# Kernel optimization log

Hardware: AMD Instinct MI355X
Metric: run time of the kernel (lower is better)

Reference implementation:

```python
import jax, jax.numpy as jnp
import numpy as np

N = 50000      # nodes
E = 800000     # edges (avg degree 16)
F_IN = 128     # input features
HID = 64       # hidden per head
HEADS = 4      # heads per layer
G = 256        # graphs in batch
C = 10         # classes
ALPHA = 0.01   # leaky relu negative slope


def setup_inputs() -> dict:
    key = jax.random.key(0)
    ks = jax.random.split(key, 12)
    x = jax.random.normal(ks[0], (N, F_IN), dtype=jnp.float32)
    edge_index = jax.random.randint(ks[1], (2, E), 0, N, dtype=jnp.int32)
    batch = jnp.sort(jax.random.randint(ks[2], (N,), 0, G, dtype=jnp.int32))

    def glorot(k, shape):
        fan_in = shape[0] if len(shape) == 2 else int(np.prod(shape[1:]))
        return (jax.random.normal(k, shape, dtype=jnp.float32) / np.float32(np.sqrt(fan_in)))

    W1 = glorot(ks[3], (F_IN, HEADS * HID))
    a1_src = glorot(ks[4], (HEADS, HID))
    a1_dst = glorot(ks[5], (HEADS, HID))
    W2 = glorot(ks[6], (HEADS * HID, HEADS * HID))
    a2_src = glorot(ks[7], (HEADS, HID))
    a2_dst = glorot(ks[8], (HEADS, HID))
    lin_W = glorot(ks[9], (2 * HEADS * HID, C))
    lin_b = jnp.zeros((C,), dtype=jnp.float32)
    return {
        "x": x, "edge_index": edge_index, "batch": batch,
        "W1": W1, "a1_src": a1_src, "a1_dst": a1_dst,
        "W2": W2, "a2_src": a2_src, "a2_dst": a2_dst,
        "lin_W": lin_W, "lin_b": lin_b,
    }


def _gat_layer(x, src, dst, W, a_src, a_dst):
    """Multi-head GAT layer: edge softmax over incoming neighbors, concat heads, ELU."""
    n = x.shape[0]
    h, f = a_src.shape
    Wh = (x @ W).reshape(n, h, f)                       # [N,H,F]
    # per-node attention logits (decomposed GAT attention a^T [Wh_i || Wh_j])
    ls = jnp.einsum("nhf,hf->nh", Wh, a_src)            # [N,H]
    ld = jnp.einsum("nhf,hf->nh", Wh, a_dst)            # [N,H]
    e = jax.nn.leaky_relu(ls[src] + ld[dst], ALPHA)      # [E,H]
    # numerically-stable softmax over edges grouped by destination node
    m = jax.ops.segment_max(e, dst, num_segments=n)      # [N,H]
    m = jnp.where(jnp.isfinite(m), m, 0.0)
    p = jnp.exp(e - m[dst])                              # [E,H]
    z = jax.ops.segment_sum(p, dst, num_segments=n)      # [N,H]
    attn = p / (z[dst] + 1e-16)                          # [E,H]
    msg = Wh[src] * attn[:, :, None]                     # [E,H,F]
    out = jax.ops.segment_sum(msg, dst, num_segments=n)  # [N,H,F]
    return jax.nn.elu(out.reshape(n, h * f))


def reference(x, edge_index, batch, W1, a1_src, a1_dst, W2, a2_src, a2_dst, lin_W, lin_b):
    src, dst = edge_index[0], edge_index[1]
    x = _gat_layer(x, src, dst, W1, a1_src, a1_dst)
    x = _gat_layer(x, src, dst, W2, a2_src, a2_dst)
    # global max / mean pool per graph
    mx = jax.ops.segment_max(x, batch, num_segments=G)
    mx = jnp.where(jnp.isfinite(mx), mx, 0.0)
    s = jax.ops.segment_sum(x, batch, num_segments=G)
    cnt = jax.ops.segment_sum(jnp.ones((x.shape[0], 1), x.dtype), batch, num_segments=G)
    mean = s / jnp.maximum(cnt, 1.0)
    pooled = jnp.concatenate([mx, mean], axis=1)         # [G, 2*H*F]
    return pooled @ lin_W + lin_b                        # [G, C]
```

## Files before the change

### kernel.cpp

```cpp
#include <hip/hip_runtime.h>
#include <hip/hip_bf16.h>

#define NNODES 50000
#define NEDGES 800000
#define FIN    128
#define HID    64
#define HEADS  4
#define NGRAPH 256
#define NCLS   10
#define DTOT   256
#define ALPHA  0.01f
#define CAPLG  6
#define CAP    (1 << CAPLG)

typedef short bf16x8 __attribute__((ext_vector_type(8)));
typedef float f32x4  __attribute__((ext_vector_type(4)));

#define NB      ((NNODES + 255) / 256)
#define EB      ((NEDGES + 255) / 256)
#define XB      ((NNODES * FIN / 4 + 255) / 256)
#define W1B     (FIN * DTOT / 256)
#define W2B     (DTOT * DTOT / 256)

__device__ __forceinline__ ushort f2bf(float v) {
    return __bfloat16_as_ushort(__float2bfloat16(v));
}
__device__ __forceinline__ float blo(unsigned u) { return __uint_as_float(u << 16); }
__device__ __forceinline__ float bhi(unsigned u) { return __uint_as_float(u & 0xffff0000u); }

__global__ __launch_bounds__(256) void k_setup(const int* __restrict__ src, const int* __restrict__ dst,
                                               int* __restrict__ cursor, ushort* __restrict__ esrc,
                                               const int* __restrict__ batch, int* __restrict__ gstart,
                                               const float4* __restrict__ x4, ushort4* __restrict__ xbf4,
                                               const float* __restrict__ W1, ushort* __restrict__ W1t,
                                               const float* __restrict__ W2, ushort* __restrict__ W2t) {
    int b = blockIdx.x, t = threadIdx.x;
    if (b < EB) {
        int e = b * 256 + t;
        if (e < NEDGES) {
            int d = dst[e];
            int pos = atomicAdd(&cursor[d], 1);
            if (pos < CAP) esrc[(d << CAPLG) + pos] = (ushort)src[e];
        }
    } else if (b < EB + NB) {
        int i = (b - EB) * 256 + t;
        if (i >= NNODES) return;
        int bb = batch[i];
        if (i == 0) {
            for (int g = 0; g <= bb; ++g) gstart[g] = 0;
        } else {
            int pb = batch[i - 1];
            if (pb != bb) for (int g = pb + 1; g <= bb; ++g) gstart[g] = i;
        }
        if (i == NNODES - 1)
            for (int g = bb + 1; g <= NGRAPH; ++g) gstart[g] = NNODES;
    } else if (b < EB + NB + XB) {
        int i = (b - EB - NB) * 256 + t;
        if (i >= NNODES * FIN / 4) return;
        float4 v = x4[i];
        ushort4 o;
        o.x = f2bf(v.x); o.y = f2bf(v.y); o.z = f2bf(v.z); o.w = f2bf(v.w);
        xbf4[i] = o;
    } else if (b < EB + NB + XB + W1B) {
        int id = (b - EB - NB - XB) * 256 + t;
        int n = id & 255, k = id >> 8;
        W1t[n * FIN + (((k >> 3) ^ (n & 7)) << 3) + (k & 7)] = f2bf(W1[k * DTOT + n]);
    } else {
        int id = (b - EB - NB - XB - W1B) * 256 + t;
        int n = id & 255, k = id >> 8;
        W2t[n * DTOT + (((k >> 3) ^ (n & 7)) << 3) + (k & 7)] = f2bf(W2[k * DTOT + n]);
    }
}

template <int K>
__global__ __launch_bounds__(256) void k_gemm_mfma(const ushort* __restrict__ Abf,
                                                   const ushort* __restrict__ Bt,
                                                   ushort* __restrict__ Cbf,
                                                   float* __restrict__ ls,
                                                   float* __restrict__ ld_,
                                                   const float* __restrict__ a_src,
                                                   const float* __restrict__ a_dst,
                                                   int M) {
    __shared__ ushort Bl[128 * K];
    const int tid  = threadIdx.x;
    const int w    = tid >> 6;
    const int lane = tid & 63;
    const int l15  = lane & 15;
    const int quad = lane >> 4;
    const int m0 = blockIdx.y * 128;
    const int n0 = blockIdx.x * 128;
    const int hb = blockIdx.x * 2;

    {
        const uint4* sp = (const uint4*)(Bt + (size_t)n0 * K);
        uint4* dp = (uint4*)Bl;
#pragma unroll
        for (int idx = tid; idx < 128 * K / 8; idx += 256) dp[idx] = sp[idx];
    }
    __syncthreads();

    f32x4 acc[2][8];
#pragma unroll
    for (int mf = 0; mf < 2; ++mf)
#pragma unroll
        for (int nf = 0; nf < 8; ++nf)
            acc[mf][nf] = (f32x4){0.f, 0.f, 0.f, 0.f};

    const int rbase = m0 + w * 32;
    int rowA0 = rbase + l15;       if (rowA0 >= M) rowA0 = M - 1;
    int rowA1 = rbase + 16 + l15;  if (rowA1 >= M) rowA1 = M - 1;
    const ushort* pa0 = Abf + (size_t)rowA0 * K + quad * 8;
    const ushort* pa1 = Abf + (size_t)rowA1 * K + quad * 8;

#pragma unroll
    for (int ks = 0; ks < K / 32; ++ks) {
        bf16x8 a0 = *(const bf16x8*)(pa0 + ks * 32);
        bf16x8 a1 = *(const bf16x8*)(pa1 + ks * 32);
        bf16x8 bfr[8];
#pragma unroll
        for (int nf = 0; nf < 8; ++nf) {
            int n = nf * 16 + l15;
            int c = (ks * 4 + quad) ^ (n & 7);
            bfr[nf] = *(const bf16x8*)&Bl[n * K + (c << 3)];
        }
#pragma unroll
        for (int nf = 0; nf < 8; ++nf) {
            acc[0][nf] = __builtin_amdgcn_mfma_f32_16x16x32_bf16(a0, bfr[nf], acc[0][nf], 0, 0, 0);
            acc[1][nf] = __builtin_amdgcn_mfma_f32_16x16x32_bf16(a1, bfr[nf], acc[1][nf], 0, 0, 0);
        }
    }

    float as[8], ad[8];
#pragma unroll
    for (int nf = 0; nf < 8; ++nf) {
        int head = hb + (nf >> 2);
        as[nf] = a_src[head * HID + (nf & 3) * 16 + l15];
        ad[nf] = a_dst[head * HID + (nf & 3) * 16 + l15];
    }
#pragma unroll
    for (int mf = 0; mf < 2; ++mf) {
#pragma unroll
        for (int reg = 0; reg < 4; ++reg) {
            int row = rbase + mf * 16 + quad * 4 + reg;
            bool ok = row < M;
            if (ok) {
#pragma unroll
                for (int nf = 0; nf < 8; ++nf)
                    Cbf[(size_t)row * DTOT + n0 + nf * 16 + l15] = f2bf(acc[mf][nf][reg]);
            }
            float s0 = 0.f, d0 = 0.f, s1 = 0.f, d1 = 0.f;
#pragma unroll
            for (int nf = 0; nf < 4; ++nf) {
                s0 += acc[mf][nf][reg] * as[nf];
                d0 += acc[mf][nf][reg] * ad[nf];
                s1 += acc[mf][nf + 4][reg] * as[nf + 4];
                d1 += acc[mf][nf + 4][reg] * ad[nf + 4];
            }
#pragma unroll
            for (int off = 1; off < 16; off <<= 1) {
                s0 += __shfl_xor(s0, off);
                d0 += __shfl_xor(d0, off);
                s1 += __shfl_xor(s1, off);
                d1 += __shfl_xor(d1, off);
            }
            if (ok && l15 == 0) {
                ls[row * HEADS + hb]      = s0;
                ld_[row * HEADS + hb]     = d0;
                ls[row * HEADS + hb + 1]  = s1;
                ld_[row * HEADS + hb + 1] = d1;
            }
        }
    }
}

__global__ __launch_bounds__(256) void k_gat_aggr(const int* __restrict__ cnt,
                                                  const ushort* __restrict__ esrc,
                                                  const ushort* __restrict__ Whbf,
                                                  const float* __restrict__ ls,
                                                  const float* __restrict__ ld_,
                                                  ushort* __restrict__ out) {
    const int wv   = threadIdx.x >> 6;
    const int lane = threadIdx.x & 63;
    const int i    = blockIdx.x * 4 + wv;
    if (i >= NNODES) return;
    const int half = lane >> 5;
    const int l32  = lane & 31;
    const int h    = l32 >> 3;
    const int e0 = i << CAPLG;
    int deg = cnt[i]; if (deg > CAP) deg = CAP;
    const int e1 = e0 + deg;
    const float ldv = ld_[i * HEADS + h];

    float mx = -INFINITY;
    for (int e = e0 + (l32 & 7) + 8 * half; e < e1; e += 16)
        mx = fmaxf(mx, ls[(int)esrc[e] * HEADS + h]);
    mx = fmaxf(mx, __shfl_xor(mx, 1));
    mx = fmaxf(mx, __shfl_xor(mx, 2));
    mx = fmaxf(mx, __shfl_xor(mx, 4));
    mx = fmaxf(mx, __shfl_xor(mx, 32));
    float lvm = mx + ldv;
    const float M = lvm > 0.f ? lvm : ALPHA * lvm;

    float ac[8] = {};
    float z = 0.f;
    const int ch = 8 * l32;
    int e = e0 + half;
    for (; e + 6 < e1; e += 8) {
        int s0 = (int)esrc[e], s1 = (int)esrc[e + 2], s2 = (int)esrc[e + 4], s3 = (int)esrc[e + 6];
        float l0 = ls[s0 * HEADS + h] + ldv;
        float l1 = ls[s1 * HEADS + h] + ldv;
        float l2 = ls[s2 * HEADS + h] + ldv;
        float l3 = ls[s3 * HEADS + h] + ldv;
        uint4 u0 = *(const uint4*)&Whbf[(size_t)s0 * DTOT + ch];
        uint4 u1 = *(const uint4*)&Whbf[(size_t)s1 * DTOT + ch];
        uint4 u2 = *(const uint4*)&Whbf[(size_t)s2 * DTOT + ch];
        uint4 u3 = *(const uint4*)&Whbf[(size_t)s3 * DTOT + ch];
        float p0 = __expf((l0 > 0.f ? l0 : ALPHA * l0) - M);
        float p1 = __expf((l1 > 0.f ? l1 : ALPHA * l1) - M);
        float p2 = __expf((l2 > 0.f ? l2 : ALPHA * l2) - M);
        float p3 = __expf((l3 > 0.f ? l3 : ALPHA * l3) - M);
        z += p0 + p1 + p2 + p3;
        ac[0] = fmaf(p0, blo(u0.x), ac[0]); ac[1] = fmaf(p0, bhi(u0.x), ac[1]);
        ac[2] = fmaf(p0, blo(u0.y), ac[2]); ac[3] = fmaf(p0, bhi(u0.y), ac[3]);
        ac[4] = fmaf(p0, blo(u0.z), ac[4]); ac[5] = fmaf(p0, bhi(u0.z), ac[5]);
        ac[6] = fmaf(p0, blo(u0.w), ac[6]); ac[7] = fmaf(p0, bhi(u0.w), ac[7]);
        ac[0] = fmaf(p1, blo(u1.x), ac[0]); ac[1] = fmaf(p1, bhi(u1.x), ac[1]);
        ac[2] = fmaf(p1, blo(u1.y), ac[2]); ac[3] = fmaf(p1, bhi(u1.y), ac[3]);
        ac[4] = fmaf(p1, blo(u1.z), ac[4]); ac[5] = fmaf(p1, bhi(u1.z), ac[5]);
        ac[6] = fmaf(p1, blo(u1.w), ac[6]); ac[7] = fmaf(p1, bhi(u1.w), ac[7]);
        ac[0] = fmaf(p2, blo(u2.x), ac[0]); ac[1] = fmaf(p2, bhi(u2.x), ac[1]);
        ac[2] = fmaf(p2, blo(u2.y), ac[2]); ac[3] = fmaf(p2, bhi(u2.y), ac[3]);
        ac[4] = fmaf(p2, blo(u2.z), ac[4]); ac[5] = fmaf(p2, bhi(u2.z), ac[5]);
        ac[6] = fmaf(p2, blo(u2.w), ac[6]); ac[7] = fmaf(p2, bhi(u2.w), ac[7]);
        ac[0] = fmaf(p3, blo(u3.x), ac[0]); ac[1] = fmaf(p3, bhi(u3.x), ac[1]);
        ac[2] = fmaf(p3, blo(u3.y), ac[2]); ac[3] = fmaf(p3, bhi(u3.y), ac[3]);
        ac[4] = fmaf(p3, blo(u3.z), ac[4]); ac[5] = fmaf(p3, bhi(u3.z), ac[5]);
        ac[6] = fmaf(p3, blo(u3.w), ac[6]); ac[7] = fmaf(p3, bhi(u3.w), ac[7]);
    }
    for (; e < e1; e += 2) {
        int s0 = (int)esrc[e];
        float l0 = ls[s0 * HEADS + h] + ldv;
        uint4 u0 = *(const uint4*)&Whbf[(size_t)s0 * DTOT + ch];
        float p0 = __expf((l0 > 0.f ? l0 : ALPHA * l0) - M);
        z += p0;
        ac[0] = fmaf(p0, blo(u0.x), ac[0]); ac[1] = fmaf(p0, bhi(u0.x), ac[1]);
        ac[2] = fmaf(p0, blo(u0.y), ac[2]); ac[3] = fmaf(p0, bhi(u0.y), ac[3]);
        ac[4] = fmaf(p0, blo(u0.z), ac[4]); ac[5] = fmaf(p0, bhi(u0.z), ac[5]);
        ac[6] = fmaf(p0, blo(u0.w), ac[6]); ac[7] = fmaf(p0, bhi(u0.w), ac[7]);
    }

#pragma unroll
    for (int j = 0; j < 8; ++j) ac[j] += __shfl_xor(ac[j], 32);
    z += __shfl_xor(z, 32);

    if (half == 0) {
        const float inv = 1.f / (z + 1e-16f);
        float v[8];
#pragma unroll
        for (int j = 0; j < 8; ++j) {
            float t = ac[j] * inv;
            v[j] = t > 0.f ? t : __expf(t) - 1.f;
        }
        ushort4 pk, pk2;
        pk.x  = f2bf(v[0]); pk.y  = f2bf(v[1]); pk.z  = f2bf(v[2]); pk.w  = f2bf(v[3]);
        pk2.x = f2bf(v[4]); pk2.y = f2bf(v[5]); pk2.z = f2bf(v[6]); pk2.w = f2bf(v[7]);
        *(ushort4*)(out + (size_t)i * DTOT + ch)     = pk;
        *(ushort4*)(out + (size_t)i * DTOT + ch + 4) = pk2;
    }
}

__global__ __launch_bounds__(1024) void k_pool_final(const ushort* __restrict__ h2bf,
                                                     const int* __restrict__ gstart,
                                                     const float* __restrict__ W,
                                                     const float* __restrict__ b,
                                                     float* __restrict__ out) {
    __shared__ float smx[4][256];
    __shared__ float ssm[4][256];
    __shared__ float pooled[2 * DTOT];
    int g = blockIdx.x, t = threadIdx.x;
    int c = t & 255, j = t >> 8;
    int s = gstart[g], e = gstart[g + 1];
    float mx = -INFINITY, sm = 0.f;
    for (int n = s + j; n < e; n += 4) {
        float vv = __uint_as_float(((unsigned)h2bf[(size_t)n * DTOT + c]) << 16);
        mx = fmaxf(mx, vv);
        sm += vv;
    }
    smx[j][c] = mx;
    ssm[j][c] = sm;
    __syncthreads();
    if (t < 256) {
        float m = fmaxf(fmaxf(smx[0][t], smx[1][t]), fmaxf(smx[2][t], smx[3][t]));
        float su = ssm[0][t] + ssm[1][t] + ssm[2][t] + ssm[3][t];
        int cnt = e - s;
        if (cnt <= 0) m = 0.f;
        pooled[t] = m;
        pooled[DTOT + t] = su / (float)(cnt > 0 ? cnt : 1);
    }
    __syncthreads();
    int wv = t >> 6, lane = t & 63;
    if (wv < NCLS) {
        float acc = 0.f;
        for (int k = lane; k < 2 * DTOT; k += 64)
            acc += pooled[k] * W[k * NCLS + wv];
#pragma unroll
        for (int off = 32; off; off >>= 1) acc += __shfl_down(acc, off);
        if (lane == 0)
            out[g * NCLS + wv] = acc + b[wv];
    }
}

extern "C" void kernel_launch(void* const* d_in, const int* in_sizes, int n_in,
                              void* d_out, int out_size, void* d_ws, size_t ws_size,
                              hipStream_t stream) {
    const float* x     = (const float*)d_in[0];
    const int*   ei    = (const int*)d_in[1];
    const int*   batch = (const int*)d_in[2];
    const float* W1    = (const float*)d_in[3];
    const float* a1s   = (const float*)d_in[4];
    const float* a1d   = (const float*)d_in[5];
    const float* W2    = (const float*)d_in[6];
    const float* a2s   = (const float*)d_in[7];
    const float* a2d   = (const float*)d_in[8];
    const float* linW  = (const float*)d_in[9];
    const float* linb  = (const float*)d_in[10];
    float* out = (float*)d_out;

    const int* src = ei;
    const int* dst = ei + NEDGES;

    size_t off = 0;
    char* base = (char*)d_ws;
    auto alloc = [&](size_t bytes) -> void* {
        void* p = base + off;
        off += (bytes + 255) & ~(size_t)255;
        return p;
    };
    ushort* xbf    = (ushort*)alloc((size_t)NNODES * FIN * 2);
    ushort* Whbf   = (ushort*)alloc((size_t)NNODES * DTOT * 2);
    ushort* h1bf   = (ushort*)alloc((size_t)NNODES * DTOT * 2);
    ushort* h2bf   = (ushort*)alloc((size_t)NNODES * DTOT * 2);
    float*  ls     = (float*)alloc((size_t)NNODES * HEADS * 4);
    float*  ld_    = (float*)alloc((size_t)NNODES * HEADS * 4);
    int*    cursor = (int*)alloc((size_t)NNODES * 4);
    ushort* esrc   = (ushort*)alloc((size_t)(NNODES << CAPLG) * 2);
    int*    gstart = (int*)alloc((size_t)(NGRAPH + 1) * 4);
    ushort* W1t    = (ushort*)alloc((size_t)DTOT * FIN * 2);
    ushort* W2t    = (ushort*)alloc((size_t)DTOT * DTOT * 2);

    hipMemsetAsync(cursor, 0, (size_t)NNODES * 4, stream);

    int setup_blocks = EB + NB + XB + W1B + W2B;
    k_setup<<<setup_blocks, 256, 0, stream>>>(src, dst, cursor, esrc, batch, gstart,
                                              (const float4*)x, (ushort4*)xbf,
                                              W1, W1t, W2, W2t);

    dim3 ggrid(2, (NNODES + 127) / 128);

    k_gemm_mfma<FIN><<<ggrid, 256, 0, stream>>>(xbf, W1t, Whbf, ls, ld_, a1s, a1d, NNODES);
    k_gat_aggr<<<(NNODES + 3) / 4, 256, 0, stream>>>(cursor, esrc, Whbf, ls, ld_, h1bf);

    k_gemm_mfma<DTOT><<<ggrid, 256, 0, stream>>>(h1bf, W2t, Whbf, ls, ld_, a2s, a2d, NNODES);
    k_gat_aggr<<<(NNODES + 3) / 4, 256, 0, stream>>>(cursor, esrc, Whbf, ls, ld_, h2bf);

    k_pool_final<<<NGRAPH, 1024, 0, stream>>>(h2bf, gstart, linW, linb, out);
}
```

Baseline: 320.9 us.

## Chunk GEMM B staging, deepen aggregation unroll with packed FMA, vectorize pooling

The GEMM now stages B into LDS in 128-wide K chunks, which caps shared memory at 32KB for the K=256 layer and may raise occupancy, at the cost of an extra barrier per chunk. The aggregation loop now issues 8 gathers before any math and accumulates with two-wide float FMAs, so more loads are in flight and the packed FMA instruction can be used. The output store becomes a single 16-byte write. Pooling reads 16-byte vectors per thread (8 channels, 32 node rows per block) instead of 2-byte scalars, and combines partials across waves through shared memory.

```diff
diff --git a/kernel.cpp b/kernel.cpp
--- a/kernel.cpp
+++ b/kernel.cpp
@@ -15,6 +15,7 @@
 
 typedef short bf16x8 __attribute__((ext_vector_type(8)));
 typedef float f32x4  __attribute__((ext_vector_type(4)));
+typedef float f32x2  __attribute__((ext_vector_type(2)));
 
 #define NB      ((NNODES + 255) / 256)
 #define EB      ((NEDGES + 255) / 256)
@@ -27,6 +28,12 @@
 }
 __device__ __forceinline__ float blo(unsigned u) { return __uint_as_float(u << 16); }
 __device__ __forceinline__ float bhi(unsigned u) { return __uint_as_float(u & 0xffff0000u); }
+__device__ __forceinline__ f32x2 bfpair(unsigned u) {
+    return (f32x2){__uint_as_float(u << 16), __uint_as_float(u & 0xffff0000u)};
+}
+__device__ __forceinline__ unsigned pack2(float lo, float hi) {
+    return ((unsigned)f2bf(hi) << 16) | (unsigned)f2bf(lo);
+}
 
 __global__ __launch_bounds__(256) void k_setup(const int* __restrict__ src, const int* __restrict__ dst,
                                                int* __restrict__ cursor, ushort* __restrict__ esrc,
@@ -81,7 +88,7 @@
                                                    const float* __restrict__ a_src,
                                                    const float* __restrict__ a_dst,
                                                    int M) {
-    __shared__ ushort Bl[128 * K];
+    __shared__ ushort Bl[128 * 128];
     const int tid  = threadIdx.x;
     const int w    = tid >> 6;
     const int lane = tid & 63;
@@ -91,14 +98,6 @@
     const int n0 = blockIdx.x * 128;
     const int hb = blockIdx.x * 2;
 
-    {
-        const uint4* sp = (const uint4*)(Bt + (size_t)n0 * K);
-        uint4* dp = (uint4*)Bl;
-#pragma unroll
-        for (int idx = tid; idx < 128 * K / 8; idx += 256) dp[idx] = sp[idx];
-    }
-    __syncthreads();
-
     f32x4 acc[2][8];
 #pragma unroll
     for (int mf = 0; mf < 2; ++mf)
@@ -113,21 +112,35 @@
     const ushort* pa1 = Abf + (size_t)rowA1 * K + quad * 8;
 
 #pragma unroll
-    for (int ks = 0; ks < K / 32; ++ks) {
-        bf16x8 a0 = *(const bf16x8*)(pa0 + ks * 32);
-        bf16x8 a1 = *(const bf16x8*)(pa1 + ks * 32);
-        bf16x8 bfr[8];
-#pragma unroll
-        for (int nf = 0; nf < 8; ++nf) {
-            int n = nf * 16 + l15;
-            int c = (ks * 4 + quad) ^ (n & 7);
-            bfr[nf] = *(const bf16x8*)&Bl[n * K + (c << 3)];
-        }
-#pragma unroll
-        for (int nf = 0; nf < 8; ++nf) {
-            acc[0][nf] = __builtin_amdgcn_mfma_f32_16x16x32_bf16(a0, bfr[nf], acc[0][nf], 0, 0, 0);
-            acc[1][nf] = __builtin_amdgcn_mfma_f32_16x16x32_bf16(a1, bfr[nf], acc[1][nf], 0, 0, 0);
-        }
+    for (int kc = 0; kc < K / 128; ++kc) {
+        {
+            const ushort* bsrc = Bt + (size_t)n0 * K + kc * 128;
+#pragma unroll
+            for (int idx = tid; idx < 2048; idx += 256) {
+                int row = idx >> 4, c16 = idx & 15;
+                *(uint4*)&Bl[row * 128 + c16 * 8] =
+                    *(const uint4*)&bsrc[(size_t)row * K + c16 * 8];
+            }
+        }
+        __syncthreads();
+#pragma unroll
+        for (int ks = 0; ks < 4; ++ks) {
+            bf16x8 a0 = *(const bf16x8*)(pa0 + kc * 128 + ks * 32);
+            bf16x8 a1 = *(const bf16x8*)(pa1 + kc * 128 + ks * 32);
+            bf16x8 bfr[8];
+#pragma unroll
+            for (int nf = 0; nf < 8; ++nf) {
+                int n = nf * 16 + l15;
+                int c = (ks * 4 + quad) ^ (n & 7);
+                bfr[nf] = *(const bf16x8*)&Bl[n * 128 + (c << 3)];
+            }
+#pragma unroll
+            for (int nf = 0; nf < 8; ++nf) {
+                acc[0][nf] = __builtin_amdgcn_mfma_f32_16x16x32_bf16(a0, bfr[nf], acc[0][nf], 0, 0, 0);
+                acc[1][nf] = __builtin_amdgcn_mfma_f32_16x16x32_bf16(a1, bfr[nf], acc[1][nf], 0, 0, 0);
+            }
+        }
+        __syncthreads();
     }
 
     float as[8], ad[8];
@@ -201,41 +214,58 @@
     float lvm = mx + ldv;
     const float M = lvm > 0.f ? lvm : ALPHA * lvm;
 
-    float ac[8] = {};
+    f32x2 ac2[4];
+#pragma unroll
+    for (int j = 0; j < 4; ++j) ac2[j] = (f32x2){0.f, 0.f};
     float z = 0.f;
     const int ch = 8 * l32;
+
     int e = e0 + half;
+    for (; e + 14 < e1; e += 16) {
+        int sb[8];
+#pragma unroll
+        for (int k = 0; k < 8; ++k) sb[k] = (int)esrc[e + 2 * k];
+        uint4 ub[8];
+        float lv[8];
+#pragma unroll
+        for (int k = 0; k < 8; ++k) {
+            ub[k] = *(const uint4*)&Whbf[(size_t)sb[k] * DTOT + ch];
+            lv[k] = ls[sb[k] * HEADS + h] + ldv;
+        }
+#pragma unroll
+        for (int k = 0; k < 8; ++k) {
+            float l = lv[k];
+            float p = __expf((l > 0.f ? l : ALPHA * l) - M);
+            z += p;
+            f32x2 pp = {p, p};
+            ac2[0] = __builtin_elementwise_fma(pp, bfpair(ub[k].x), ac2[0]);
+            ac2[1] = __builtin_elementwise_fma(pp, bfpair(ub[k].y), ac2[1]);
+            ac2[2] = __builtin_elementwise_fma(pp, bfpair(ub[k].z), ac2[2]);
+            ac2[3] = __builtin_elementwise_fma(pp, bfpair(ub[k].w), ac2[3]);
+        }
+    }
     for (; e + 6 < e1; e += 8) {
-        int s0 = (int)esrc[e], s1 = (int)esrc[e + 2], s2 = (int)esrc[e + 4], s3 = (int)esrc[e + 6];
-        float l0 = ls[s0 * HEADS + h] + ldv;
-        float l1 = ls[s1 * HEADS + h] + ldv;
-        float l2 = ls[s2 * HEADS + h] + ldv;
-        float l3 = ls[s3 * HEADS + h] + ldv;
-        uint4 u0 = *(const uint4*)&Whbf[(size_t)s0 * DTOT + ch];
-        uint4 u1 = *(const uint4*)&Whbf[(size_t)s1 * DTOT + ch];
-        uint4 u2 = *(const uint4*)&Whbf[(size_t)s2 * DTOT + ch];
-        uint4 u3 = *(const uint4*)&Whbf[(size_t)s3 * DTOT + ch];
-        float p0 = __expf((l0 > 0.f ? l0 : ALPHA * l0) - M);
-        float p1 = __expf((l1 > 0.f ? l1 : ALPHA * l1) - M);
-        float p2 = __expf((l2 > 0.f ? l2 : ALPHA * l2) - M);
-        float p3 = __expf((l3 > 0.f ? l3 : ALPHA * l3) - M);
-        z += p0 + p1 + p2 + p3;
-        ac[0] = fmaf(p0, blo(u0.x), ac[0]); ac[1] = fmaf(p0, bhi(u0.x), ac[1]);
-        ac[2] = fmaf(p0, blo(u0.y), ac[2]); ac[3] = fmaf(p0, bhi(u0.y), ac[3]);
-        ac[4] = fmaf(p0, blo(u0.z), ac[4]); ac[5] = fmaf(p0, bhi(u0.z), ac[5]);
-        ac[6] = fmaf(p0, blo(u0.w), ac[6]); ac[7] = fmaf(p0, bhi(u0.w), ac[7]);
-        ac[0] = fmaf(p1, blo(u1.x), ac[0]); ac[1] = fmaf(p1, bhi(u1.x), ac[1]);
-        ac[2] = fmaf(p1, blo(u1.y), ac[2]); ac[3] = fmaf(p1, bhi(u1.y), ac[3]);
-        ac[4] = fmaf(p1, blo(u1.z), ac[4]); ac[5] = fmaf(p1, bhi(u1.z), ac[5]);
-        ac[6] = fmaf(p1, blo(u1.w), ac[6]); ac[7] = fmaf(p1, bhi(u1.w), ac[7]);
-        ac[0] = fmaf(p2, blo(u2.x), ac[0]); ac[1] = fmaf(p2, bhi(u2.x), ac[1]);
-        ac[2] = fmaf(p2, blo(u2.y), ac[2]); ac[3] = fmaf(p2, bhi(u2.y), ac[3]);
-        ac[4] = fmaf(p2, blo(u2.z), ac[4]); ac[5] = fmaf(p2, bhi(u2.z), ac[5]);
-        ac[6] = fmaf(p2, blo(u2.w), ac[6]); ac[7] = fmaf(p2, bhi(u2.w), ac[7]);
-        ac[0] = fmaf(p3, blo(u3.x), ac[0]); ac[1] = fmaf(p3, bhi(u3.x), ac[1]);
-        ac[2] = fmaf(p3, blo(u3.y), ac[2]); ac[3] = fmaf(p3, bhi(u3.y), ac[3]);
-        ac[4] = fmaf(p3, blo(u3.z), ac[4]); ac[5] = fmaf(p3, bhi(u3.z), ac[5]);
-        ac[6] = fmaf(p3, blo(u3.w), ac[6]); ac[7] = fmaf(p3, bhi(u3.w), ac[7]);
+        int sb[4];
+#pragma unroll
+        for (int k = 0; k < 4; ++k) sb[k] = (int)esrc[e + 2 * k];
+        uint4 ub[4];
+        float lv[4];
+#pragma unroll
+        for (int k = 0; k < 4; ++k) {
+            ub[k] = *(const uint4*)&Whbf[(size_t)sb[k] * DTOT + ch];
+            lv[k] = ls[sb[k] * HEADS + h] + ldv;
+        }
+#pragma unroll
+        for (int k = 0; k < 4; ++k) {
+            float l = lv[k];
+            float p = __expf((l > 0.f ? l : ALPHA * l) - M);
+            z += p;
+            f32x2 pp = {p, p};
+            ac2[0] = __builtin_elementwise_fma(pp, bfpair(ub[k].x), ac2[0]);
+            ac2[1] = __builtin_elementwise_fma(pp, bfpair(ub[k].y), ac2[1]);
+            ac2[2] = __builtin_elementwise_fma(pp, bfpair(ub[k].z), ac2[2]);
+            ac2[3] = __builtin_elementwise_fma(pp, bfpair(ub[k].w), ac2[3]);
+        }
     }
     for (; e < e1; e += 2) {
         int s0 = (int)esrc[e];
@@ -243,29 +273,35 @@
         uint4 u0 = *(const uint4*)&Whbf[(size_t)s0 * DTOT + ch];
         float p0 = __expf((l0 > 0.f ? l0 : ALPHA * l0) - M);
         z += p0;
-        ac[0] = fmaf(p0, blo(u0.x), ac[0]); ac[1] = fmaf(p0, bhi(u0.x), ac[1]);
-        ac[2] = fmaf(p0, blo(u0.y), ac[2]); ac[3] = fmaf(p0, bhi(u0.y), ac[3]);
-        ac[4] = fmaf(p0, blo(u0.z), ac[4]); ac[5] = fmaf(p0, bhi(u0.z), ac[5]);
-        ac[6] = fmaf(p0, blo(u0.w), ac[6]); ac[7] = fmaf(p0, bhi(u0.w), ac[7]);
-    }
-
-#pragma unroll
-    for (int j = 0; j < 8; ++j) ac[j] += __shfl_xor(ac[j], 32);
+        f32x2 pp0 = {p0, p0};
+        ac2[0] = __builtin_elementwise_fma(pp0, bfpair(u0.x), ac2[0]);
+        ac2[1] = __builtin_elementwise_fma(pp0, bfpair(u0.y), ac2[1]);
+        ac2[2] = __builtin_elementwise_fma(pp0, bfpair(u0.z), ac2[2]);
+        ac2[3] = __builtin_elementwise_fma(pp0, bfpair(u0.w), ac2[3]);
+    }
+
+#pragma unroll
+    for (int j = 0; j < 4; ++j) {
+        ac2[j][0] += __shfl_xor(ac2[j][0], 32);
+        ac2[j][1] += __shfl_xor(ac2[j][1], 32);
+    }
     z += __shfl_xor(z, 32);
 
     if (half == 0) {
         const float inv = 1.f / (z + 1e-16f);
         float v[8];
 #pragma unroll
-        for (int j = 0; j < 8; ++j) {
-            float t = ac[j] * inv;
-            v[j] = t > 0.f ? t : __expf(t) - 1.f;
-        }
-        ushort4 pk, pk2;
-        pk.x  = f2bf(v[0]); pk.y  = f2bf(v[1]); pk.z  = f2bf(v[2]); pk.w  = f2bf(v[3]);
-        pk2.x = f2bf(v[4]); pk2.y = f2bf(v[5]); pk2.z = f2bf(v[6]); pk2.w = f2bf(v[7]);
-        *(ushort4*)(out + (size_t)i * DTOT + ch)     = pk;
-        *(ushort4*)(out + (size_t)i * DTOT + ch + 4) = pk2;
+        for (int j = 0; j < 4; ++j) {
+            float t0 = ac2[j][0] * inv, t1 = ac2[j][1] * inv;
+            v[2 * j]     = t0 > 0.f ? t0 : __expf(t0) - 1.f;
+            v[2 * j + 1] = t1 > 0.f ? t1 : __expf(t1) - 1.f;
+        }
+        uint4 pk;
+        pk.x = pack2(v[0], v[1]);
+        pk.y = pack2(v[2], v[3]);
+        pk.z = pack2(v[4], v[5]);
+        pk.w = pack2(v[6], v[7]);
+        *(uint4*)(out + (size_t)i * DTOT + ch) = pk;
     }
 }
 
@@ -274,31 +310,55 @@
                                                      const float* __restrict__ W,
                                                      const float* __restrict__ b,
                                                      float* __restrict__ out) {
-    __shared__ float smx[4][256];
-    __shared__ float ssm[4][256];
+    __shared__ float smx[16][256];
+    __shared__ float ssm[16][256];
     __shared__ float pooled[2 * DTOT];
     int g = blockIdx.x, t = threadIdx.x;
-    int c = t & 255, j = t >> 8;
+    int cg = t & 31, j = t >> 5;
     int s = gstart[g], e = gstart[g + 1];
-    float mx = -INFINITY, sm = 0.f;
-    for (int n = s + j; n < e; n += 4) {
-        float vv = __uint_as_float(((unsigned)h2bf[(size_t)n * DTOT + c]) << 16);
-        mx = fmaxf(mx, vv);
-        sm += vv;
-    }
-    smx[j][c] = mx;
-    ssm[j][c] = sm;
+    float mx[8], sm[8];
+#pragma unroll
+    for (int k = 0; k < 8; ++k) { mx[k] = -INFINITY; sm[k] = 0.f; }
+    for (int n = s + j; n < e; n += 32) {
+        uint4 u = *(const uint4*)&h2bf[(size_t)n * DTOT + cg * 8];
+        float v0 = blo(u.x), v1 = bhi(u.x), v2 = blo(u.y), v3 = bhi(u.y);
+        float v4 = blo(u.z), v5 = bhi(u.z), v6 = blo(u.w), v7 = bhi(u.w);
+        mx[0] = fmaxf(mx[0], v0); sm[0] += v0;
+        mx[1] = fmaxf(mx[1], v1); sm[1] += v1;
+        mx[2] = fmaxf(mx[2], v2); sm[2] += v2;
+        mx[3] = fmaxf(mx[3], v3); sm[3] += v3;
+        mx[4] = fmaxf(mx[4], v4); sm[4] += v4;
+        mx[5] = fmaxf(mx[5], v5); sm[5] += v5;
+        mx[6] = fmaxf(mx[6], v6); sm[6] += v6;
+        mx[7] = fmaxf(mx[7], v7); sm[7] += v7;
+    }
+#pragma unroll
+    for (int k = 0; k < 8; ++k) {
+        mx[k] = fmaxf(mx[k], __shfl_xor(mx[k], 32));
+        sm[k] += __shfl_xor(sm[k], 32);
+    }
+    int wave = t >> 6, lane = t & 63;
+    if (lane < 32) {
+        *(float4*)&smx[wave][lane * 8]     = make_float4(mx[0], mx[1], mx[2], mx[3]);
+        *(float4*)&smx[wave][lane * 8 + 4] = make_float4(mx[4], mx[5], mx[6], mx[7]);
+        *(float4*)&ssm[wave][lane * 8]     = make_float4(sm[0], sm[1], sm[2], sm[3]);
+        *(float4*)&ssm[wave][lane * 8 + 4] = make_float4(sm[4], sm[5], sm[6], sm[7]);
+    }
     __syncthreads();
     if (t < 256) {
-        float m = fmaxf(fmaxf(smx[0][t], smx[1][t]), fmaxf(smx[2][t], smx[3][t]));
-        float su = ssm[0][t] + ssm[1][t] + ssm[2][t] + ssm[3][t];
+        float m = -INFINITY, su = 0.f;
+#pragma unroll
+        for (int jj = 0; jj < 16; ++jj) {
+            m = fmaxf(m, smx[jj][t]);
+            su += ssm[jj][t];
+        }
         int cnt = e - s;
         if (cnt <= 0) m = 0.f;
         pooled[t] = m;
         pooled[DTOT + t] = su / (float)(cnt > 0 ? cnt : 1);
     }
     __syncthreads();
-    int wv = t >> 6, lane = t & 63;
+    int wv = t >> 6;
     if (wv < NCLS) {
         float acc = 0.f;
         for (int k = lane; k < 2 * DTOT; k += 64)
```

Measured after the change: 326.1 us. About the same (+1.6%).
